# Performance work log

Hardware: AMD Instinct MI355X
Metric: run time of the kernel (lower is better)

Reference implementation:

```python
import jax, jax.numpy as jnp
import numpy as np

N = 50000      # nodes
E = 800000     # edges (avg degree 16)
LM = 768       # lm_input_dim
H = 192        # hidden_dim = 32*6
B6 = 32        # per-branch dim = hidden_dim/6
SLOPE = 0.01   # nn.LeakyReLU default negative slope


def setup_inputs() -> dict:
    key = jax.random.key(0)
    ks = jax.random.split(key, 32)
    f = lambda i, shape, s=0.05: (jax.random.normal(ks[i], shape, jnp.float32) * s)
    inp = {
        "pre_x": f(0, (N, LM)),
        "x": f(1, (N, LM)),
        "edge_index": jax.random.randint(ks[2], (2, E), 0, N),
        "edge_type": jax.random.randint(ks[3], (E,), 0, 3),
        "num_prop": f(4, (N, 5)),
        "num_category": f(5, (N, 1)),
        "des_tensor": f(6, (N, LM)),
        "tweet_tensor": f(7, (N, LM)),
        # parameters (torch nn.Linear convention: W is [out, in], y = x @ W.T + b)
        "W_des": f(8, (B6, LM)), "b_des": f(9, (B6,)),
        "W_tweet": f(10, (B6, LM)), "b_tweet": f(11, (B6,)),
        "W_tweet_tr": f(12, (B6, LM)), "b_tweet_tr": f(13, (B6,)),
        "W_prop": f(14, (B6, 5)), "b_prop": f(15, (B6,)),
        "W_cat": f(16, (B6, 1)), "b_cat": f(17, (B6,)),
        "W_text": f(18, (B6, LM)), "b_text": f(19, (B6,)),
        "W_in": f(20, (H, H)), "b_in": f(21, (H,)),
        "W_c1": f(22, (H, H)), "b_c1": f(23, (H,)),
        "W_c2": f(24, (H, H)), "b_c2": f(25, (H,)),
        "W_o1": f(26, (96, H)), "b_o1": f(27, (96,)),
        "W_o2": f(28, (2, 96)), "b_o2": f(29, (2,)),
    }
    return inp


def _gcn_conv(h, W, b, src, dst):
    """PyG GCNConv: symmetric-normalized aggregation with added self-loops.
    out[v] = sum_{u->v} (d_u d_v)^{-1/2} (h_u W^T) + (1/d_v) (h_v W^T) + b
    where d includes the self-loop (+1)."""
    n = h.shape[0]
    hW = h @ W.T                                                  # [N, H]
    deg = jax.ops.segment_sum(jnp.ones(src.shape[0], h.dtype), dst,
                              num_segments=n) + 1.0               # [N]
    dinv = jax.lax.rsqrt(deg)
    norm = dinv[src] * dinv[dst]                                  # [E]
    agg = jax.ops.segment_sum(hW[src] * norm[:, None], dst,
                              num_segments=n)                     # [N, H]
    return agg + hW * (1.0 / deg)[:, None] + b


def reference(pre_x, x, edge_index, edge_type, num_prop, num_category,
              des_tensor, tweet_tensor,
              W_des, b_des, W_tweet, b_tweet, W_tweet_tr, b_tweet_tr,
              W_prop, b_prop, W_cat, b_cat, W_text, b_text,
              W_in, b_in, W_c1, b_c1, W_c2, b_c2,
              W_o1, b_o1, W_o2, b_o2):
    lrelu = lambda v: jax.nn.leaky_relu(v, SLOPE)
    branch = lambda t, W, b: lrelu(t @ W.T + b)   # dropout is identity in eval

    d = branch(des_tensor, W_des, b_des)
    pre_t = branch(pre_x, W_tweet, b_tweet)
    t = branch(x, W_tweet_tr, b_tweet_tr)
    n = branch(num_prop, W_prop, b_prop)
    c = branch(num_category, W_cat, b_cat)
    tw = branch(tweet_tensor, W_text, b_text)

    h = jnp.concatenate((n, c, d, tw, pre_t, t), axis=1)          # [N, 192]
    h = lrelu(h @ W_in.T + b_in)

    src, dst = edge_index[0], edge_index[1]
    h = _gcn_conv(h, W_c1, b_c1, src, dst)
    h = _gcn_conv(h, W_c2, b_c2, src, dst)

    em = lrelu(h @ W_o1.T + b_o1)                                 # [N, 96]
    out = em @ W_o2.T + b_o2                                      # [N, 2]
    return (out, em)
```

## Files before the change

### kernel.cpp

```cpp
#include <hip/hip_runtime.h>

#define NN 50000
#define EE 800000
#define LMD 768
#define HD 192
#define SLOPE 0.01f

typedef short bf16x8 __attribute__((ext_vector_type(8)));
typedef float f32x4 __attribute__((ext_vector_type(4)));
typedef unsigned short u16;

__device__ __forceinline__ float lrelu(float v){ return v > 0.f ? v : SLOPE * v; }

__device__ __forceinline__ u16 f2bf(float f){
    unsigned u = __float_as_uint(f);
    u += 0x7FFF + ((u >> 16) & 1u);
    return (u16)(u >> 16);
}
__device__ __forceinline__ float bf2f(u16 v){
    return __uint_as_float(((unsigned)v) << 16);
}
__device__ __forceinline__ bf16x8 as_bf8(float4 v){
    union { float4 f; bf16x8 b; } u; u.f = v; return u.b;
}

#define GLOAD16(gp, lp) __builtin_amdgcn_global_load_lds( \
    (const __attribute__((address_space(1))) void*)(gp), \
    (__attribute__((address_space(3))) void*)(lp), 16, 0, 0)

__global__ __launch_bounds__(256) void k_prep(
    const float* __restrict__ W0, const float* __restrict__ W1,
    const float* __restrict__ W2, const float* __restrict__ W3,
    const float* __restrict__ Win, const float* __restrict__ Wc1,
    const float* __restrict__ Wc2, const float* __restrict__ Wo1,
    u16* __restrict__ out)
{
    int m = blockIdx.y;
    int idx = blockIdx.x * 256 + threadIdx.x;
    const float* src; int nelem; int K;
    switch (m) {
      case 0: src = W0;  nelem = 32*768;  K = 768; break;
      case 1: src = W1;  nelem = 32*768;  K = 768; break;
      case 2: src = W2;  nelem = 32*768;  K = 768; break;
      case 3: src = W3;  nelem = 32*768;  K = 768; break;
      case 4: src = Win; nelem = 192*192; K = 192; break;
      case 5: src = Wc1; nelem = 192*192; K = 192; break;
      case 6: src = Wc2; nelem = 192*192; K = 192; break;
      default: src = Wo1; nelem = 96*192; K = 192; break;
    }
    if (idx >= nelem) return;
    u16 v = f2bf(src[idx]);
    int c = idx / K, k = idx - c * K;
    int cb = c >> 4, lr = c & 15;
    int sg = k >> 5, kk = k & 31, hi = kk >> 3, j = kk & 7;
    int lane = hi * 16 + lr;
    size_t dst;
    if (m < 4)      dst = (size_t)m * 24576 + (sg * 2 + cb) * 512 + lane * 8 + j;
    else if (m < 7) dst = 98304 + (size_t)(m - 4) * 36864 + (sg * 12 + cb) * 512 + lane * 8 + j;
    else            dst = 208896 + (size_t)(sg * 6 + cb) * 512 + lane * 8 + j;
    out[dst] = v;
}

__global__ __launch_bounds__(256) void k_branch(
    const float* __restrict__ des, const float* __restrict__ twt,
    const float* __restrict__ prex, const float* __restrict__ xx,
    const u16* __restrict__ Wf,
    const float* __restrict__ bd, const float* __restrict__ btx,
    const float* __restrict__ btw, const float* __restrict__ btr,
    u16* __restrict__ h)
{
    __shared__ u16 Ws_[24576];
    __shared__ float Ab[3][64][32];

    const int br = blockIdx.y;
    const float* A; const float* bias; int colBase;
    switch (br) {
      case 0:  A = des;  bias = bd;  colBase = 64;  break;
      case 1:  A = twt;  bias = btx; colBase = 96;  break;
      case 2:  A = prex; bias = btw; colBase = 128; break;
      default: A = xx;   bias = btr; colBase = 160; break;
    }

    const int t = threadIdx.x, w = t >> 6, l = t & 63;
    const int hi = l >> 4, lr = l & 15;
    const int rowBase = blockIdx.x * 64;

    {
        const uint4* s_ = (const uint4*)(Wf + br * 24576);
        uint4* d_ = (uint4*)Ws_;
        #pragma unroll
        for (int i = 0; i < 12; ++i) d_[i * 256 + t] = s_[i * 256 + t];
    }
    __syncthreads();

    const int rl_ = w * 16 + (l >> 3);
    const int s16 = l & 7, g_ = s16 >> 1, hf = s16 & 1;

#define STAGE(cc, bufi) { \
    _Pragma("unroll") for (int i_ = 0; i_ < 2; ++i_) { \
        int rl = rl_ + i_ * 8; \
        int rg = rowBase + rl; if (rg >= NN) rg = NN - 1; \
        const float* gp = A + (size_t)rg * LMD + (cc) * 32 + ((g_ ^ (rl & 3)) * 8 + hf * 4); \
        GLOAD16(gp, &Ab[bufi][w * 16 + i_ * 8][0]); } }

    STAGE(0, 0);
    STAGE(1, 1);

    f32x4 acc[2] = {};

    #pragma unroll
    for (int c = 0; c < 24; ++c) {
        if (c + 2 < 24) {
            const int bufi = (c + 2) % 3;
            STAGE(c + 2, bufi);
        }
        if (c < 22)      { asm volatile("s_waitcnt vmcnt(4)" ::: "memory"); }
        else if (c == 22){ asm volatile("s_waitcnt vmcnt(2)" ::: "memory"); }
        else             { asm volatile("s_waitcnt vmcnt(0)" ::: "memory"); }
        __builtin_amdgcn_sched_barrier(0);

        const float* ab = &Ab[c % 3][w * 16 + lr][(hi ^ (lr & 3)) * 8];
        float4 lo = *(const float4*)ab;
        float4 hp = *(const float4*)(ab + 4);
        bf16x8 af;
        af[0] = (short)f2bf(lo.x); af[1] = (short)f2bf(lo.y);
        af[2] = (short)f2bf(lo.z); af[3] = (short)f2bf(lo.w);
        af[4] = (short)f2bf(hp.x); af[5] = (short)f2bf(hp.y);
        af[6] = (short)f2bf(hp.z); af[7] = (short)f2bf(hp.w);
        #pragma unroll
        for (int cb = 0; cb < 2; ++cb) {
            bf16x8 bf = *(const bf16x8*)(Ws_ + (c * 2 + cb) * 512 + l * 8);
            acc[cb] = __builtin_amdgcn_mfma_f32_16x16x32_bf16(af, bf, acc[cb], 0, 0, 0);
        }
    }
#undef STAGE

    #pragma unroll
    for (int cb = 0; cb < 2; ++cb) {
        int cl = cb * 16 + lr;
        float bv = bias[cl];
        #pragma unroll
        for (int rg = 0; rg < 4; ++rg) {
            int r = rowBase + w * 16 + hi * 4 + rg;
            if (r < NN)
                h[(size_t)r * HD + colBase + cl] = f2bf(lrelu(acc[cb][rg] + bv));
        }
    }
}

template<bool BIAS, bool LRELU>
__global__ __launch_bounds__(512) void k_hgemm(
    const u16* __restrict__ A, const u16* __restrict__ Wf,
    const float* __restrict__ bias, u16* __restrict__ out)
{
    __shared__ u16 Bs[36864];
    const int t = threadIdx.x, w = t >> 6, l = t & 63;
    const int hi = l >> 4, lr = l & 15;
    const int rowBase = blockIdx.x * 128;
    {
        const uint4* s_ = (const uint4*)Wf; uint4* d_ = (uint4*)Bs;
        #pragma unroll
        for (int i = 0; i < 9; ++i) d_[i * 512 + t] = s_[i * 512 + t];
    }
    int r0 = rowBase + w * 16 + lr;
    int rowc = r0 < NN ? r0 : NN - 1;
    const u16* ap = A + (size_t)rowc * HD;
    float4 araw[6];
    #pragma unroll
    for (int sg = 0; sg < 6; ++sg) {
        araw[sg] = *(const float4*)(ap + sg * 32 + hi * 8);
        asm volatile("" :: "v"(araw[sg].x), "v"(araw[sg].y), "v"(araw[sg].z), "v"(araw[sg].w));
    }
    __syncthreads();

    f32x4 acc[12] = {};
    #pragma unroll
    for (int sg = 0; sg < 6; ++sg) {
        bf16x8 af = as_bf8(araw[sg]);
        #pragma unroll
        for (int cb = 0; cb < 12; ++cb) {
            bf16x8 bf = *(const bf16x8*)(Bs + (sg * 12 + cb) * 512 + l * 8);
            acc[cb] = __builtin_amdgcn_mfma_f32_16x16x32_bf16(af, bf, acc[cb], 0, 0, 0);
        }
    }

    #pragma unroll
    for (int cb = 0; cb < 12; ++cb) {
        int cl = cb * 16 + lr;
        float bv = BIAS ? bias[cl] : 0.f;
        #pragma unroll
        for (int rg = 0; rg < 4; ++rg) {
            int r = rowBase + w * 16 + hi * 4 + rg;
            if (r < NN) {
                float v = acc[cb][rg] + bv;
                if (LRELU) v = lrelu(v);
                out[(size_t)r * HD + cl] = f2bf(v);
            }
        }
    }
}

__global__ __launch_bounds__(512) void k_final(
    const u16* __restrict__ A, const u16* __restrict__ Wf,
    const float* __restrict__ b1, const float* __restrict__ W2,
    const float* __restrict__ b2, float* __restrict__ em, float* __restrict__ out)
{
    __shared__ u16 Bs[18432];
    const int t = threadIdx.x, w = t >> 6, l = t & 63;
    const int hi = l >> 4, lr = l & 15;
    const int rowBase = blockIdx.x * 128;
    {
        const uint4* s_ = (const uint4*)Wf; uint4* d_ = (uint4*)Bs;
        #pragma unroll
        for (int i = 0; i < 5; ++i) { int idx = i * 512 + t; if (idx < 2304) d_[idx] = s_[idx]; }
    }
    int r0 = rowBase + w * 16 + lr;
    int rowc = r0 < NN ? r0 : NN - 1;
    const u16* ap = A + (size_t)rowc * HD;
    float4 araw[6];
    #pragma unroll
    for (int sg = 0; sg < 6; ++sg) {
        araw[sg] = *(const float4*)(ap + sg * 32 + hi * 8);
        asm volatile("" :: "v"(araw[sg].x), "v"(araw[sg].y), "v"(araw[sg].z), "v"(araw[sg].w));
    }
    __syncthreads();

    f32x4 acc[6] = {};
    #pragma unroll
    for (int sg = 0; sg < 6; ++sg) {
        bf16x8 af = as_bf8(araw[sg]);
        #pragma unroll
        for (int cb = 0; cb < 6; ++cb) {
            bf16x8 bf = *(const bf16x8*)(Bs + (sg * 6 + cb) * 512 + l * 8);
            acc[cb] = __builtin_amdgcn_mfma_f32_16x16x32_bf16(af, bf, acc[cb], 0, 0, 0);
        }
    }

    float w2v[2][6], bv[6];
    #pragma unroll
    for (int cb = 0; cb < 6; ++cb) {
        bv[cb] = b1[cb * 16 + lr];
        w2v[0][cb] = W2[cb * 16 + lr];
        w2v[1][cb] = W2[96 + cb * 16 + lr];
    }

    #pragma unroll
    for (int rg = 0; rg < 4; ++rg) {
        int r = rowBase + w * 16 + hi * 4 + rg;
        float o0 = 0.f, o1 = 0.f;
        #pragma unroll
        for (int cb = 0; cb < 6; ++cb) {
            float v = lrelu(acc[cb][rg] + bv[cb]);
            if (r < NN) em[(size_t)r * 96 + cb * 16 + lr] = v;
            o0 += v * w2v[0][cb];
            o1 += v * w2v[1][cb];
        }
        #pragma unroll
        for (int d = 1; d < 16; d <<= 1) {
            o0 += __shfl_xor(o0, d);
            o1 += __shfl_xor(o1, d);
        }
        if (lr == 0 && r < NN) {
            out[r * 2 + 0] = o0 + b2[0];
            out[r * 2 + 1] = o1 + b2[1];
        }
    }
}

__global__ __launch_bounds__(256) void k_small_branch(
    const float* __restrict__ nprop, const float* __restrict__ ncat,
    const float* __restrict__ Wp, const float* __restrict__ bp,
    const float* __restrict__ Wc, const float* __restrict__ bc,
    u16* __restrict__ h)
{
    int idx = blockIdx.x * 256 + threadIdx.x;
    if (idx >= NN * 64) return;
    int row = idx >> 6, c = idx & 63;
    float acc;
    if (c < 32) {
        acc = bp[c];
        #pragma unroll
        for (int k = 0; k < 5; ++k) acc += nprop[row * 5 + k] * Wp[c * 5 + k];
    } else {
        int cc = c - 32;
        acc = bc[cc] + ncat[row] * Wc[cc];
    }
    h[(size_t)row * HD + c] = f2bf(lrelu(acc));
}

__global__ void k_count(const int* __restrict__ ei, int* __restrict__ deg)
{
    int e = blockIdx.x * 256 + threadIdx.x;
    if (e < EE) atomicAdd(&deg[ei[EE + e]], 1);
}

__global__ void k_deginv(const int* __restrict__ deg, float* __restrict__ dinv, float* __restrict__ invdeg)
{
    int v = blockIdx.x * 256 + threadIdx.x;
    if (v < NN) {
        float d = (float)(deg[v] + 1);
        dinv[v] = rsqrtf(d);
        invdeg[v] = 1.0f / d;
    }
}

__global__ __launch_bounds__(1024) void k_scan1(const int* __restrict__ deg, int* __restrict__ rp, int* __restrict__ part)
{
    __shared__ int sh[1024];
    int tid = threadIdx.x, i = blockIdx.x * 1024 + tid;
    int x = (i < NN) ? deg[i] : 0;
    sh[tid] = x;
    __syncthreads();
    for (int off = 1; off < 1024; off <<= 1) {
        int y = (tid >= off) ? sh[tid - off] : 0;
        __syncthreads();
        sh[tid] += y;
        __syncthreads();
    }
    if (i < NN) rp[i] = sh[tid] - x;
    if (tid == 1023) part[blockIdx.x] = sh[tid];
}

__global__ void k_scan2(int* part, int nb, int* rp)
{
    if (threadIdx.x == 0 && blockIdx.x == 0) {
        int run = 0;
        for (int b = 0; b < nb; ++b) { int t = part[b]; part[b] = run; run += t; }
        rp[NN] = run;
    }
}

__global__ void k_scan3(int* rp, const int* __restrict__ part)
{
    int i = blockIdx.x * 256 + threadIdx.x;
    if (i < NN) rp[i] += part[i >> 10];
}

__global__ void k_fill(const int* __restrict__ ei, const float* __restrict__ dinv,
                       int* __restrict__ cursor, int* __restrict__ cs, float* __restrict__ nrm)
{
    int e = blockIdx.x * 256 + threadIdx.x;
    if (e >= EE) return;
    int s = ei[e], d = ei[EE + e];
    int pos = atomicAdd(&cursor[d], 1);
    cs[pos] = s;
    nrm[pos] = dinv[s] * dinv[d];
}

__global__ __launch_bounds__(240) void k_agg(const u16* __restrict__ hW,
    const int* __restrict__ rp, const int* __restrict__ cs, const float* __restrict__ nrm,
    const float* __restrict__ invdeg, const float* __restrict__ bias, u16* __restrict__ out)
{
    int v = blockIdx.x * 5 + threadIdx.y;
    int f0 = threadIdx.x * 4;
    int s0 = rp[v], s1 = rp[v + 1];
    float4 bv = *reinterpret_cast<const float4*>(bias + f0);
    ushort4 hv = *reinterpret_cast<const ushort4*>(hW + (size_t)v * HD + f0);
    float idg = invdeg[v];
    float a0 = bf2f(hv.x) * idg + bv.x;
    float a1 = bf2f(hv.y) * idg + bv.y;
    float a2 = bf2f(hv.z) * idg + bv.z;
    float a3 = bf2f(hv.w) * idg + bv.w;
    int i = s0;
    for (; i + 4 <= s1; i += 4) {
        int c0 = cs[i], c1 = cs[i+1], c2 = cs[i+2], c3 = cs[i+3];
        float n0 = nrm[i], n1 = nrm[i+1], n2 = nrm[i+2], n3 = nrm[i+3];
        ushort4 g0 = *reinterpret_cast<const ushort4*>(hW + (size_t)c0 * HD + f0);
        ushort4 g1 = *reinterpret_cast<const ushort4*>(hW + (size_t)c1 * HD + f0);
        ushort4 g2 = *reinterpret_cast<const ushort4*>(hW + (size_t)c2 * HD + f0);
        ushort4 g3 = *reinterpret_cast<const ushort4*>(hW + (size_t)c3 * HD + f0);
        a0 += bf2f(g0.x) * n0; a1 += bf2f(g0.y) * n0; a2 += bf2f(g0.z) * n0; a3 += bf2f(g0.w) * n0;
        a0 += bf2f(g1.x) * n1; a1 += bf2f(g1.y) * n1; a2 += bf2f(g1.z) * n1; a3 += bf2f(g1.w) * n1;
        a0 += bf2f(g2.x) * n2; a1 += bf2f(g2.y) * n2; a2 += bf2f(g2.z) * n2; a3 += bf2f(g2.w) * n2;
        a0 += bf2f(g3.x) * n3; a1 += bf2f(g3.y) * n3; a2 += bf2f(g3.z) * n3; a3 += bf2f(g3.w) * n3;
    }
    for (; i < s1; ++i) {
        int c = cs[i]; float n = nrm[i];
        ushort4 g = *reinterpret_cast<const ushort4*>(hW + (size_t)c * HD + f0);
        a0 += bf2f(g.x) * n; a1 += bf2f(g.y) * n; a2 += bf2f(g.z) * n; a3 += bf2f(g.w) * n;
    }
    ushort4 o;
    o.x = f2bf(a0); o.y = f2bf(a1); o.z = f2bf(a2); o.w = f2bf(a3);
    *reinterpret_cast<ushort4*>(out + (size_t)v * HD + f0) = o;
}

extern "C" void kernel_launch(void* const* d_in, const int* in_sizes, int n_in,
                              void* d_out, int out_size, void* d_ws, size_t ws_size,
                              hipStream_t stream)
{
    const float* pre_x = (const float*)d_in[0];
    const float* x     = (const float*)d_in[1];
    const int*   ei    = (const int*)d_in[2];
    const float* nprop = (const float*)d_in[4];
    const float* ncat  = (const float*)d_in[5];
    const float* des   = (const float*)d_in[6];
    const float* twt   = (const float*)d_in[7];
    const float* W_des  = (const float*)d_in[8],  *b_des  = (const float*)d_in[9];
    const float* W_tw   = (const float*)d_in[10], *b_tw   = (const float*)d_in[11];
    const float* W_tr   = (const float*)d_in[12], *b_tr   = (const float*)d_in[13];
    const float* W_prop = (const float*)d_in[14], *b_prop = (const float*)d_in[15];
    const float* W_cat  = (const float*)d_in[16], *b_cat  = (const float*)d_in[17];
    const float* W_text = (const float*)d_in[18], *b_text = (const float*)d_in[19];
    const float* W_in   = (const float*)d_in[20], *b_in   = (const float*)d_in[21];
    const float* W_c1   = (const float*)d_in[22], *b_c1   = (const float*)d_in[23];
    const float* W_c2   = (const float*)d_in[24], *b_c2   = (const float*)d_in[25];
    const float* W_o1   = (const float*)d_in[26], *b_o1   = (const float*)d_in[27];
    const float* W_o2   = (const float*)d_in[28], *b_o2   = (const float*)d_in[29];

    char* base = (char*)d_ws;
    size_t off = 0;
    auto alloc = [&](size_t bytes) -> char* {
        char* p = base + off;
        off = (off + bytes + 255) & ~(size_t)255;
        return p;
    };
    u16*   hA     = (u16*)alloc((size_t)NN * HD * 2);
    u16*   hB     = (u16*)alloc((size_t)NN * HD * 2);
    u16*   hC     = (u16*)alloc((size_t)NN * HD * 2);
    u16*   Wprep  = (u16*)alloc((size_t)227328 * 2);
    float* dinv   = (float*)alloc((size_t)NN * 4);
    float* invdeg = (float*)alloc((size_t)NN * 4);
    int*   deg    = (int*)alloc((size_t)NN * 4);
    int*   rp     = (int*)alloc((size_t)(NN + 1) * 4);
    int*   cursor = (int*)alloc((size_t)NN * 4);
    int*   part   = (int*)alloc(64 * 4);
    int*   cs     = (int*)alloc((size_t)EE * 4);
    float* nrm    = (float*)alloc((size_t)EE * 4);
    (void)ws_size; (void)in_sizes; (void)n_in; (void)out_size;

    float* outp = (float*)d_out;
    float* em   = outp + (size_t)NN * 2;

    const int rb     = (NN + 255) / 256;
    const int rb64   = (NN + 63) / 64;
    const int rb128  = (NN + 127) / 128;
    const int eb     = (EE + 255) / 256;
    const int nb1024 = (NN + 1023) / 1024;

    hipMemsetAsync(deg, 0, (size_t)NN * 4, stream);
    hipLaunchKernelGGL(k_prep, dim3(144, 8), dim3(256), 0, stream,
        W_des, W_text, W_tw, W_tr, W_in, W_c1, W_c2, W_o1, Wprep);
    hipLaunchKernelGGL(k_count,  dim3(eb), dim3(256), 0, stream, ei, deg);
    hipLaunchKernelGGL(k_deginv, dim3(rb), dim3(256), 0, stream, deg, dinv, invdeg);
    hipLaunchKernelGGL(k_scan1,  dim3(nb1024), dim3(1024), 0, stream, deg, rp, part);
    hipLaunchKernelGGL(k_scan2,  dim3(1), dim3(1), 0, stream, part, nb1024, rp);
    hipLaunchKernelGGL(k_scan3,  dim3(rb), dim3(256), 0, stream, rp, part);
    hipMemcpyAsync(cursor, rp, (size_t)NN * 4, hipMemcpyDeviceToDevice, stream);
    hipLaunchKernelGGL(k_fill,   dim3(eb), dim3(256), 0, stream, ei, dinv, cursor, cs, nrm);

    hipLaunchKernelGGL(k_branch, dim3(rb64, 4), dim3(256), 0, stream,
        des, twt, pre_x, x, Wprep, b_des, b_text, b_tw, b_tr, hA);
    hipLaunchKernelGGL(k_small_branch, dim3((NN * 64 + 255) / 256), dim3(256), 0, stream,
        nprop, ncat, W_prop, b_prop, W_cat, b_cat, hA);

    hipLaunchKernelGGL((k_hgemm<true, true>),   dim3(rb128), dim3(512), 0, stream,
        hA, Wprep + 98304, b_in, hB);
    hipLaunchKernelGGL((k_hgemm<false, false>), dim3(rb128), dim3(512), 0, stream,
        hB, Wprep + 98304 + 36864, nullptr, hC);
    hipLaunchKernelGGL(k_agg, dim3(NN / 5), dim3(48, 5), 0, stream, hC, rp, cs, nrm, invdeg, b_c1, hA);
    hipLaunchKernelGGL((k_hgemm<false, false>), dim3(rb128), dim3(512), 0, stream,
        hA, Wprep + 98304 + 2 * 36864, nullptr, hB);
    hipLaunchKernelGGL(k_agg, dim3(NN / 5), dim3(48, 5), 0, stream, hB, rp, cs, nrm, invdeg, b_c2, hC);

    hipLaunchKernelGGL(k_final, dim3(rb128), dim3(512), 0, stream,
        hC, Wprep + 208896, b_o1, W_o2, b_o2, em, outp);
}
```

Before: 405.3 us.

## Rewrite branch GEMM as persistent split-K kernel with register weights and prefetch

The four 768-wide branch projections now run as a persistent grid of 192x4 blocks that loop over 16-row tiles. Each wave holds its quarter of the weight fragments in registers instead of LDS. Whole rows are loaded with coalesced float4 global reads, one tile ahead in registers, converted to bf16 into LDS, and the K split across waves is reduced through an LDS scratch buffer. The aim is more bytes in flight and less LDS traffic on this bandwidth-bound stage, at the cost of two block barriers per small tile, higher register pressure, and a hardcoded tile count that assumes N divisible by 16.

Result: no change. 399.1 us (-1.5%).

```diff
diff --git a/kernel.cpp b/kernel.cpp
--- a/kernel.cpp
+++ b/kernel.cpp
@@ -23,10 +23,6 @@
 __device__ __forceinline__ bf16x8 as_bf8(float4 v){
     union { float4 f; bf16x8 b; } u; u.f = v; return u.b;
 }
-
-#define GLOAD16(gp, lp) __builtin_amdgcn_global_load_lds( \
-    (const __attribute__((address_space(1))) void*)(gp), \
-    (__attribute__((address_space(3))) void*)(lp), 16, 0, 0)
 
 __global__ __launch_bounds__(256) void k_prep(
     const float* __restrict__ W0, const float* __restrict__ W1,
@@ -61,7 +57,7 @@
     out[dst] = v;
 }
 
-__global__ __launch_bounds__(256) void k_branch(
+__global__ __launch_bounds__(256, 3) void k_branch(
     const float* __restrict__ des, const float* __restrict__ twt,
     const float* __restrict__ prex, const float* __restrict__ xx,
     const u16* __restrict__ Wf,
@@ -69,8 +65,8 @@
     const float* __restrict__ btw, const float* __restrict__ btr,
     u16* __restrict__ h)
 {
-    __shared__ u16 Ws_[24576];
-    __shared__ float Ab[3][64][32];
+    __shared__ u16 Abuf[16][776];
+    __shared__ float scr[4][16][32];
 
     const int br = blockIdx.y;
     const float* A; const float* bias; int colBase;
@@ -81,70 +77,74 @@
       default: A = xx;   bias = btr; colBase = 160; break;
     }
 
-    const int t = threadIdx.x, w = t >> 6, l = t & 63;
+    const int t0 = threadIdx.x, w = t0 >> 6, l = t0 & 63;
     const int hi = l >> 4, lr = l & 15;
-    const int rowBase = blockIdx.x * 64;
-
+
+    bf16x8 Bfr[12];
     {
-        const uint4* s_ = (const uint4*)(Wf + br * 24576);
-        uint4* d_ = (uint4*)Ws_;
-        #pragma unroll
-        for (int i = 0; i < 12; ++i) d_[i * 256 + t] = s_[i * 256 + t];
-    }
-    __syncthreads();
-
-    const int rl_ = w * 16 + (l >> 3);
-    const int s16 = l & 7, g_ = s16 >> 1, hf = s16 & 1;
-
-#define STAGE(cc, bufi) { \
-    _Pragma("unroll") for (int i_ = 0; i_ < 2; ++i_) { \
-        int rl = rl_ + i_ * 8; \
-        int rg = rowBase + rl; if (rg >= NN) rg = NN - 1; \
-        const float* gp = A + (size_t)rg * LMD + (cc) * 32 + ((g_ ^ (rl & 3)) * 8 + hf * 4); \
-        GLOAD16(gp, &Ab[bufi][w * 16 + i_ * 8][0]); } }
-
-    STAGE(0, 0);
-    STAGE(1, 1);
-
-    f32x4 acc[2] = {};
-
-    #pragma unroll
-    for (int c = 0; c < 24; ++c) {
-        if (c + 2 < 24) {
-            const int bufi = (c + 2) % 3;
-            STAGE(c + 2, bufi);
-        }
-        if (c < 22)      { asm volatile("s_waitcnt vmcnt(4)" ::: "memory"); }
-        else if (c == 22){ asm volatile("s_waitcnt vmcnt(2)" ::: "memory"); }
-        else             { asm volatile("s_waitcnt vmcnt(0)" ::: "memory"); }
-        __builtin_amdgcn_sched_barrier(0);
-
-        const float* ab = &Ab[c % 3][w * 16 + lr][(hi ^ (lr & 3)) * 8];
-        float4 lo = *(const float4*)ab;
-        float4 hp = *(const float4*)(ab + 4);
-        bf16x8 af;
-        af[0] = (short)f2bf(lo.x); af[1] = (short)f2bf(lo.y);
-        af[2] = (short)f2bf(lo.z); af[3] = (short)f2bf(lo.w);
-        af[4] = (short)f2bf(hp.x); af[5] = (short)f2bf(hp.y);
-        af[6] = (short)f2bf(hp.z); af[7] = (short)f2bf(hp.w);
-        #pragma unroll
-        for (int cb = 0; cb < 2; ++cb) {
-            bf16x8 bf = *(const bf16x8*)(Ws_ + (c * 2 + cb) * 512 + l * 8);
-            acc[cb] = __builtin_amdgcn_mfma_f32_16x16x32_bf16(af, bf, acc[cb], 0, 0, 0);
-        }
-    }
-#undef STAGE
-
-    #pragma unroll
-    for (int cb = 0; cb < 2; ++cb) {
-        int cl = cb * 16 + lr;
-        float bv = bias[cl];
-        #pragma unroll
-        for (int rg = 0; rg < 4; ++rg) {
-            int r = rowBase + w * 16 + hi * 4 + rg;
-            if (r < NN)
-                h[(size_t)r * HD + colBase + cl] = f2bf(lrelu(acc[cb][rg] + bv));
-        }
+        const u16* wp = Wf + br * 24576;
+        #pragma unroll
+        for (int cc = 0; cc < 6; ++cc)
+            #pragma unroll
+            for (int cb = 0; cb < 2; ++cb)
+                Bfr[cc * 2 + cb] = *(const bf16x8*)(wp + ((w * 6 + cc) * 2 + cb) * 512 + l * 8);
+    }
+
+    const int rrow = t0 >> 4;
+    const int col0 = (t0 & 15) * 2;
+    const float bias0 = bias[col0], bias1 = bias[col0 + 1];
+
+    float4 f4[12];
+    int tile = blockIdx.x;
+    {
+        const float* ab = A + (size_t)tile * 12288 + w * 3072 + l * 4;
+        #pragma unroll
+        for (int i = 0; i < 12; ++i) f4[i] = *(const float4*)(ab + i * 256);
+    }
+
+    for (; tile < 3125; tile += 192) {
+        asm volatile("s_waitcnt vmcnt(0)" ::: "memory");
+        #pragma unroll
+        for (int i = 0; i < 12; ++i) {
+            const int rr = i / 3, third = i % 3;
+            unsigned plo = (unsigned)f2bf(f4[i].x) | ((unsigned)f2bf(f4[i].y) << 16);
+            unsigned phi = (unsigned)f2bf(f4[i].z) | ((unsigned)f2bf(f4[i].w) << 16);
+            uint2 pk; pk.x = plo; pk.y = phi;
+            *(uint2*)&Abuf[w * 4 + rr][third * 256 + l * 4] = pk;
+        }
+        const int tnext = tile + 192;
+        if (tnext < 3125) {
+            const float* ab = A + (size_t)tnext * 12288 + w * 3072 + l * 4;
+            #pragma unroll
+            for (int i = 0; i < 12; ++i) f4[i] = *(const float4*)(ab + i * 256);
+        }
+        __syncthreads();
+
+        f32x4 acc[2] = {};
+        #pragma unroll
+        for (int cc = 0; cc < 6; ++cc) {
+            const int cg = w * 6 + cc;
+            bf16x8 af = *(const bf16x8*)&Abuf[lr][cg * 32 + hi * 8];
+            acc[0] = __builtin_amdgcn_mfma_f32_16x16x32_bf16(af, Bfr[cc * 2 + 0], acc[0], 0, 0, 0);
+            acc[1] = __builtin_amdgcn_mfma_f32_16x16x32_bf16(af, Bfr[cc * 2 + 1], acc[1], 0, 0, 0);
+        }
+        #pragma unroll
+        for (int cb = 0; cb < 2; ++cb)
+            #pragma unroll
+            for (int rg = 0; rg < 4; ++rg)
+                scr[w][hi * 4 + rg][cb * 16 + lr] = acc[cb][rg];
+        __syncthreads();
+
+        float2 s; s.x = 0.f; s.y = 0.f;
+        #pragma unroll
+        for (int ww = 0; ww < 4; ++ww) {
+            float2 p = *(const float2*)&scr[ww][rrow][col0];
+            s.x += p.x; s.y += p.y;
+        }
+        float v0 = lrelu(s.x + bias0);
+        float v1 = lrelu(s.y + bias1);
+        unsigned pk = (unsigned)f2bf(v0) | ((unsigned)f2bf(v1) << 16);
+        *(unsigned*)&h[((size_t)tile * 16 + rrow) * HD + colBase + col0] = pk;
     }
 }
 
@@ -432,7 +432,6 @@
     float* em   = outp + (size_t)NN * 2;
 
     const int rb     = (NN + 255) / 256;
-    const int rb64   = (NN + 63) / 64;
     const int rb128  = (NN + 127) / 128;
     const int eb     = (EE + 255) / 256;
     const int nb1024 = (NN + 1023) / 1024;
@@ -448,7 +447,7 @@
     hipMemcpyAsync(cursor, rp, (size_t)NN * 4, hipMemcpyDeviceToDevice, stream);
     hipLaunchKernelGGL(k_fill,   dim3(eb), dim3(256), 0, stream, ei, dinv, cursor, cs, nrm);
 
-    hipLaunchKernelGGL(k_branch, dim3(rb64, 4), dim3(256), 0, stream,
+    hipLaunchKernelGGL(k_branch, dim3(192, 4), dim3(256), 0, stream,
         des, twt, pre_x, x, Wprep, b_des, b_text, b_tw, b_tr, hA);
     hipLaunchKernelGGL(k_small_branch, dim3((NN * 64 + 255) / 256), dim3(256), 0, stream,
         nprop, ncat, W_prop, b_prop, W_cat, b_cat, hA);
```
